# Optimization experiments

Hardware: AMD Instinct MI355X
Metric: run time of the kernel (lower is better)

The kernel has to match this reference:

```python
import jax, jax.numpy as jnp
import numpy as np

C = 66  # channels (joints)
NB_CLASSES = 14
T = 96


def conv1d(x, w, b, pad, groups=1):
    # x: (N, Cin, L), w: (Cout, Cin//groups, K)
    y = jax.lax.conv_general_dilated(
        x, w, window_strides=(1,), padding=[(pad, pad)],
        feature_group_count=groups, dimension_numbers=('NCH', 'OIH', 'NCH'))
    return y + b[None, :, None]


def pool2(x):
    # AvgPool1d(kernel_size=2) along last axis
    return x.reshape(*x.shape[:-1], x.shape[-1] // 2, 2).mean(-1)


def setup_inputs() -> dict:
    key = jax.random.key(0)
    ks = jax.random.split(key, 16)

    def xavier(k, shape, fan_in, fan_out, gain=jnp.sqrt(2.0)):
        bound = gain * jnp.sqrt(6.0 / (fan_in + fan_out))
        return jax.random.uniform(k, shape, jnp.float32, -bound, bound)

    B = 2048
    x = jax.random.normal(ks[0], (B, T, C), jnp.float32)
    # shared convs (same weights for every channel)
    w_hs = xavier(ks[1], (8, 1, 7), 1 * 7, 8 * 7)
    b_hs = jnp.full((8,), 0.1, jnp.float32)
    w_ls = xavier(ks[2], (8, 1, 3), 1 * 3, 8 * 3)
    b_ls = jnp.full((8,), 0.1, jnp.float32)
    # per-channel individual convs, packed for grouped conv (groups=C)
    w_hi1 = xavier(ks[3], (C * 4, 8, 7), 8 * 7, 4 * 7)
    b_hi1 = jnp.full((C * 4,), 0.1, jnp.float32)
    w_hi2 = xavier(ks[4], (C * 4, 4, 7), 4 * 7, 4 * 7)
    b_hi2 = jnp.full((C * 4,), 0.1, jnp.float32)
    w_li1 = xavier(ks[5], (C * 4, 8, 3), 8 * 3, 4 * 3)
    b_li1 = jnp.full((C * 4,), 0.1, jnp.float32)
    w_li2 = xavier(ks[6], (C * 4, 4, 3), 4 * 3, 4 * 3)
    b_li2 = jnp.full((C * 4,), 0.1, jnp.float32)
    # MLP
    F_IN = 9 * C * 12
    w_fc1 = xavier(ks[7], (1936, F_IN), F_IN, 1936)
    b_fc1 = jnp.full((1936,), 0.1, jnp.float32)
    w_fc2 = xavier(ks[8], (NB_CLASSES, 1936), 1936, NB_CLASSES)
    b_fc2 = jnp.full((NB_CLASSES,), 0.1, jnp.float32)
    return dict(x=x, w_hs=w_hs, b_hs=b_hs, w_ls=w_ls, b_ls=b_ls,
                w_hi1=w_hi1, b_hi1=b_hi1, w_hi2=w_hi2, b_hi2=b_hi2,
                w_li1=w_li1, b_li1=b_li1, w_li2=w_li2, b_li2=b_li2,
                w_fc1=w_fc1, b_fc1=b_fc1, w_fc2=w_fc2, b_fc2=b_fc2)


def _branch(xc_flat, B, w_s, b_s, w_i1, b_i1, w_i2, b_i2, pad):
    # xc_flat: (B*C, 1, T). Shared conv applied per channel, then grouped
    # (per-channel) convs with groups=C.
    h = pool2(jax.nn.relu(conv1d(xc_flat, w_s, b_s, pad)))       # (B*C, 8, 48)
    h = h.reshape(B, C * 8, T // 2)
    h = pool2(jax.nn.relu(conv1d(h, w_i1, b_i1, pad, groups=C)))  # (B, C*4, 24)
    h = pool2(jax.nn.relu(conv1d(h, w_i2, b_i2, pad, groups=C)))  # (B, C*4, 12)
    return h.reshape(B, C, 4, T // 8)


def reference(x, w_hs, b_hs, w_ls, b_ls, w_hi1, b_hi1, w_hi2, b_hi2,
              w_li1, b_li1, w_li2, b_li2, w_fc1, b_fc1, w_fc2, b_fc2):
    B = x.shape[0]
    xc = jnp.transpose(x, (0, 2, 1))            # (B, C, T)
    xc_flat = xc.reshape(B * C, 1, T)
    high = _branch(xc_flat, B, w_hs, b_hs, w_hi1, b_hi1, w_hi2, b_hi2, pad=3)
    low = _branch(xc_flat, B, w_ls, b_ls, w_li1, b_li1, w_li2, b_li2, pad=1)
    orig = pool2(pool2(pool2(xc)))[:, :, None, :]  # (B, C, 1, 12)
    # per-channel concat order: [original, low, high] -> (B, C, 9, 12)
    feat = jnp.concatenate([orig, low, high], axis=2).reshape(B, 9 * C * 12)
    h = jax.nn.relu(feat @ w_fc1.T + b_fc1)
    return h @ w_fc2.T + b_fc2
```

## Files before the change

kernel.cpp:

```cpp
#include <hip/hip_runtime.h>
#include <hip/hip_bf16.h>

#define T_LEN 96
#define C_CH  66
#define FIN   7128
#define KPAD  7168
#define NFC1  1936
#define NPAD  2048
#define NCLS  14

typedef __bf16 bf16x8 __attribute__((ext_vector_type(8)));
typedef float  f32x4  __attribute__((ext_vector_type(4)));

#define GLD_LDS(gp, lp) __builtin_amdgcn_global_load_lds(                     \
    (__attribute__((address_space(1))) void*)(gp),                            \
    (__attribute__((address_space(3))) void*)(lp), 16, 0, 0)

__global__ __launch_bounds__(256) void transpose_kernel(
    const float* __restrict__ x, float* __restrict__ xT, int B)
{
    __shared__ float tile[64][65];
    const int t = threadIdx.x & 63;
    const int w = threadIdx.x >> 6;
    const int tc0 = blockIdx.x * 64;
    const int b0  = blockIdx.y * 64;
    #pragma unroll
    for (int j = 0; j < 16; j++) {
        const int r = w * 16 + j;
        tile[r][t] = x[(size_t)(b0 + r) * (T_LEN * C_CH) + tc0 + t];
    }
    __syncthreads();
    #pragma unroll
    for (int j = 0; j < 16; j++) {
        const int r = w * 16 + j;
        xT[(size_t)(tc0 + r) * B + b0 + t] = tile[t][r];
    }
}

__global__ __launch_bounds__(256) void pad_w_kernel(
    const float* __restrict__ w, __hip_bfloat16* __restrict__ wb)
{
    int idx = blockIdx.x * 256 + threadIdx.x;
    int row = idx / 896;
    int cc  = idx - row * 896;
    float4 a = {0.f, 0.f, 0.f, 0.f}, b = {0.f, 0.f, 0.f, 0.f};
    if (row < NFC1 && cc < 891) {
        const float4* src = (const float4*)(w + (size_t)row * FIN + cc * 8);
        a = src[0];
        b = src[1];
    }
    __align__(16) __hip_bfloat16 v[8];
    v[0] = __float2bfloat16(a.x); v[1] = __float2bfloat16(a.y);
    v[2] = __float2bfloat16(a.z); v[3] = __float2bfloat16(a.w);
    v[4] = __float2bfloat16(b.x); v[5] = __float2bfloat16(b.y);
    v[6] = __float2bfloat16(b.z); v[7] = __float2bfloat16(b.w);
    *(int4*)(wb + (size_t)row * KPAD + cc * 8) = *(const int4*)v;
}

template <int K, bool DO_EXTRA>
__device__ __forceinline__ void conv_branch(
    const float* __restrict__ xb, int ts,
    const float* __restrict__ wS, const float* __restrict__ bS,
    const float* __restrict__ wi1, const float* __restrict__ bi1,
    const float* __restrict__ wi2, const float* __restrict__ bi2,
    __hip_bfloat16* __restrict__ frow, int out_off)
{
    constexpr int PAD = K / 2;
    constexpr int XW  = 24 + 6 * PAD;
    constexpr int THW = 12 + 2 * PAD;

    float s2phR[4][24];

    #pragma unroll
    for (int tt = 0; tt < 4; tt++) {
        float xw[XW];
        #pragma unroll
        for (int i = 0; i < XW; i++) {
            const int t = 24 * tt - 3 * PAD + i;
            xw[i] = (t >= 0 && t < T_LEN) ? xb[(size_t)t * ts] : 0.f;
        }

        if (DO_EXTRA) {
            #pragma unroll
            for (int r = 0; r < 3; r++) {
                float s = 0.f;
                #pragma unroll
                for (int k = 0; k < 8; k++) s += xw[3 * PAD + 8 * r + k];
                frow[3 * tt + r] = __float2bfloat16(s * 0.125f);
            }
        }

        float s2a[4][12];
        #pragma unroll
        for (int oc = 0; oc < 4; oc++) {
            const float bv = bi1[oc];
            #pragma unroll
            for (int q = 0; q < 12; q++) s2a[oc][q] = bv;
        }

        #pragma unroll 1
        for (int ic = 0; ic < 8; ic++) {
            const float bs1 = bS[ic];
            float thw[THW];
            #pragma unroll
            for (int j = 0; j < THW; j++) {
                const int jg = 12 * tt - PAD + j;
                if (jg < 0 || jg >= 48) { thw[j] = 0.f; continue; }
                float y0 = bs1, y1 = bs1;
                #pragma unroll
                for (int k = 0; k < K; k++) {
                    const float w = wS[ic * K + k];
                    y0 = fmaf(w, xw[2 * j + k], y0);
                    y1 = fmaf(w, xw[2 * j + 1 + k], y1);
                }
                thw[j] = 0.5f * (fmaxf(y0, 0.f) + fmaxf(y1, 0.f));
            }
            #pragma unroll
            for (int q = 0; q < 12; q++) {
                #pragma unroll
                for (int oc = 0; oc < 4; oc++) {
                    float a = s2a[oc][q];
                    #pragma unroll
                    for (int k = 0; k < K; k++)
                        a = fmaf(wi1[(oc * 8 + ic) * K + k], thw[q + k], a);
                    s2a[oc][q] = a;
                }
            }
        }

        #pragma unroll
        for (int oc = 0; oc < 4; oc++)
            #pragma unroll
            for (int r = 0; r < 6; r++)
                s2phR[oc][6 * tt + r] =
                    0.5f * (fmaxf(s2a[oc][2 * r], 0.f) +
                            fmaxf(s2a[oc][2 * r + 1], 0.f));
    }

    #pragma unroll 1
    for (int oc = 0; oc < 4; oc++) {
        const float bv = bi2[oc];
        #pragma unroll
        for (int q = 0; q < 12; q++) {
            float y0 = bv, y1 = bv;
            #pragma unroll
            for (int ic = 0; ic < 4; ic++) {
                #pragma unroll
                for (int k = 0; k < K; k++) {
                    const float w = wi2[(oc * 4 + ic) * K + k];
                    const int i0 = 2 * q + k - PAD;
                    const int i1 = 2 * q + 1 + k - PAD;
                    if (i0 >= 0 && i0 < 24) y0 = fmaf(w, s2phR[ic][i0], y0);
                    if (i1 >= 0 && i1 < 24) y1 = fmaf(w, s2phR[ic][i1], y1);
                }
            }
            frow[out_off + oc * 12 + q] =
                __float2bfloat16(0.5f * (fmaxf(y0, 0.f) + fmaxf(y1, 0.f)));
        }
    }
}

__global__ __launch_bounds__(64, 2) void conv_fused_kernel(
    const float* __restrict__ x, int ts, int bs, int cs,
    const float* __restrict__ w_hs, const float* __restrict__ b_hs,
    const float* __restrict__ w_ls, const float* __restrict__ b_ls,
    const float* __restrict__ w_hi1, const float* __restrict__ b_hi1,
    const float* __restrict__ w_hi2, const float* __restrict__ b_hi2,
    const float* __restrict__ w_li1, const float* __restrict__ b_li1,
    const float* __restrict__ w_li2, const float* __restrict__ b_li2,
    __hip_bfloat16* __restrict__ feat)
{
    const int lane = threadIdx.x;
    const int b = blockIdx.x * 64 + lane;
    const int c = blockIdx.y;
    const float* xb = x + (size_t)b * bs + (size_t)c * cs;
    __hip_bfloat16* frow = feat + (size_t)b * KPAD + c * 108;

    if (blockIdx.z == 0) {
        conv_branch<7, false>(xb, ts, w_hs, b_hs,
                              w_hi1 + c * 224, b_hi1 + c * 4,
                              w_hi2 + c * 112, b_hi2 + c * 4, frow, 60);
    } else {
        if (c == 0) {
            int4* tail = (int4*)(feat + (size_t)b * KPAD + FIN);
            const int4 z = {0, 0, 0, 0};
            #pragma unroll
            for (int i = 0; i < 5; i++) tail[i] = z;
        }
        conv_branch<3, true>(xb, ts, w_ls, b_ls,
                             w_li1 + c * 96, b_li1 + c * 4,
                             w_li2 + c * 48, b_li2 + c * 4, frow, 12);
    }
}

__global__ __launch_bounds__(256) void gemm_kernel(
    const __hip_bfloat16* __restrict__ A,
    const __hip_bfloat16* __restrict__ Bw,
    float* __restrict__ Cm, int kchunk)
{
    __shared__ __align__(16) __hip_bfloat16 As[4096];
    __shared__ __align__(16) __hip_bfloat16 Bs[4096];

    const int tid  = threadIdx.x;
    const int lane = tid & 63;
    const int wid  = tid >> 6;
    const int m0 = blockIdx.y * 128;
    const int n0 = blockIdx.x * 128;
    const int wm = (wid >> 1) * 64;
    const int wn = (wid & 1) * 64;
    const int lr = lane & 15;
    const int quad = lane >> 4;

    const int r0 = tid >> 2, c0 = (tid & 3) * 8;
    const __hip_bfloat16* gA0 = A  + (size_t)(m0 + r0) * KPAD + c0;
    const __hip_bfloat16* gA1 = gA0 + (size_t)64 * KPAD;
    const __hip_bfloat16* gB0 = Bw + (size_t)(n0 + r0) * KPAD + c0;
    const __hip_bfloat16* gB1 = gB0 + (size_t)64 * KPAD;
    __hip_bfloat16* lA0 = As + wid * 512;
    __hip_bfloat16* lA1 = As + 2048 + wid * 512;
    __hip_bfloat16* lB0 = Bs + wid * 512;
    __hip_bfloat16* lB1 = Bs + 2048 + wid * 512;

    f32x4 acc[4][4] = {};

    const int kBeg = blockIdx.z * kchunk;
    const int kEnd = kBeg + kchunk;
    for (int k0 = kBeg; k0 < kEnd; k0 += 32) {
        __syncthreads();
        GLD_LDS(gA0 + k0, lA0);
        GLD_LDS(gA1 + k0, lA1);
        GLD_LDS(gB0 + k0, lB0);
        GLD_LDS(gB1 + k0, lB1);
        __syncthreads();
        bf16x8 af[4], bfr[4];
        #pragma unroll
        for (int mt = 0; mt < 4; mt++)
            af[mt] = *(const bf16x8*)(As + (wm + mt * 16 + lr) * 32 + quad * 8);
        #pragma unroll
        for (int nt = 0; nt < 4; nt++)
            bfr[nt] = *(const bf16x8*)(Bs + (wn + nt * 16 + lr) * 32 + quad * 8);
        #pragma unroll
        for (int mt = 0; mt < 4; mt++)
            #pragma unroll
            for (int nt = 0; nt < 4; nt++)
                acc[mt][nt] = __builtin_amdgcn_mfma_f32_16x16x32_bf16(
                    af[mt], bfr[nt], acc[mt][nt], 0, 0, 0);
    }

    float* Cs = Cm + (size_t)blockIdx.z * NPAD * NPAD;
    #pragma unroll
    for (int mt = 0; mt < 4; mt++) {
        #pragma unroll
        for (int nt = 0; nt < 4; nt++) {
            const int col = n0 + wn + nt * 16 + lr;
            const int rb  = m0 + wm + mt * 16 + quad * 4;
            #pragma unroll
            for (int r = 0; r < 4; r++)
                Cs[(size_t)(rb + r) * NPAD + col] = acc[mt][nt][r];
        }
    }
}

__global__ __launch_bounds__(256) void fc2_kernel(
    const float* __restrict__ h1, const float* __restrict__ b1,
    const float* __restrict__ w2, const float* __restrict__ b2,
    float* __restrict__ out, int nslab)
{
    const int b = blockIdx.x;
    const int tid = threadIdx.x;
    float acc[NCLS];
    #pragma unroll
    for (int o = 0; o < NCLS; o++) acc[o] = 0.f;
    for (int n = tid; n < NFC1; n += 256) {
        float hv = b1[n];
        for (int s = 0; s < nslab; s++)
            hv += h1[(size_t)s * NPAD * NPAD + (size_t)b * NPAD + n];
        float h = fmaxf(hv, 0.f);
        #pragma unroll
        for (int o = 0; o < NCLS; o++)
            acc[o] = fmaf(h, w2[o * NFC1 + n], acc[o]);
    }
    __shared__ float red[4][NCLS];
    #pragma unroll
    for (int o = 0; o < NCLS; o++) {
        float v = acc[o];
        #pragma unroll
        for (int s = 32; s > 0; s >>= 1) v += __shfl_down(v, s);
        if ((tid & 63) == 0) red[tid >> 6][o] = v;
    }
    __syncthreads();
    if (tid < NCLS)
        out[b * NCLS + tid] = red[0][tid] + red[1][tid] + red[2][tid] +
                              red[3][tid] + b2[tid];
}

extern "C" void kernel_launch(void* const* d_in, const int* in_sizes, int n_in,
                              void* d_out, int out_size, void* d_ws, size_t ws_size,
                              hipStream_t stream)
{
    (void)n_in; (void)out_size;
    const float* x     = (const float*)d_in[0];
    const float* w_hs  = (const float*)d_in[1];
    const float* b_hs  = (const float*)d_in[2];
    const float* w_ls  = (const float*)d_in[3];
    const float* b_ls  = (const float*)d_in[4];
    const float* w_hi1 = (const float*)d_in[5];
    const float* b_hi1 = (const float*)d_in[6];
    const float* w_hi2 = (const float*)d_in[7];
    const float* b_hi2 = (const float*)d_in[8];
    const float* w_li1 = (const float*)d_in[9];
    const float* b_li1 = (const float*)d_in[10];
    const float* w_li2 = (const float*)d_in[11];
    const float* b_li2 = (const float*)d_in[12];
    const float* w_fc1 = (const float*)d_in[13];
    const float* b_fc1 = (const float*)d_in[14];
    const float* w_fc2 = (const float*)d_in[15];
    const float* b_fc2 = (const float*)d_in[16];
    float* out = (float*)d_out;

    const int B = in_sizes[0] / (T_LEN * C_CH);

    char* ws = (char*)d_ws;
    const size_t featB = (size_t)B * KPAD * 2;
    const size_t wbB   = (size_t)NPAD * KPAD * 2;
    const size_t slabB = (size_t)NPAD * NPAD * 4;
    const size_t xtB   = (size_t)T_LEN * C_CH * B * 4;
    const size_t base2 = featB + wbB;

    __hip_bfloat16* feat = (__hip_bfloat16*)ws;
    __hip_bfloat16* wb   = (__hip_bfloat16*)(ws + featB);
    float* h1            = (float*)(ws + base2);

    const int sk = (ws_size >= base2 + 4 * slabB) ? 4 : 2;
    const bool use_xt = (ws_size >= base2 + sk * slabB + xtB);
    float* xT = (float*)(ws + base2 + sk * slabB);

    pad_w_kernel<<<dim3((NPAD * 896) / 256), 256, 0, stream>>>(w_fc1, wb);

    const float* cx = x;
    int ts = C_CH, bsi = T_LEN * C_CH, cs = 1;
    if (use_xt) {
        transpose_kernel<<<dim3(99, B / 64), 256, 0, stream>>>(x, xT, B);
        cx = xT; ts = C_CH * B; bsi = 1; cs = B;
    }
    conv_fused_kernel<<<dim3(B / 64, C_CH, 2), 64, 0, stream>>>(
        cx, ts, bsi, cs, w_hs, b_hs, w_ls, b_ls,
        w_hi1, b_hi1, w_hi2, b_hi2, w_li1, b_li1, w_li2, b_li2, feat);
    gemm_kernel<<<dim3(NPAD / 128, B / 128, sk), 256, 0, stream>>>(
        feat, wb, h1, KPAD / sk);
    fc2_kernel<<<dim3(B), 256, 0, stream>>>(h1, b_fc1, w_fc2, b_fc2, out, sk);
}
```

Before: 431.2 us.

## Stream conv stage-3 over sliding window and split branches into separate kernels

The fused conv kernel is split into two templated kernels, one per branch (K=7 and K=3), each launched separately with launch bounds raised to 3 blocks per SIMD. The time loop now processes 12-sample tiles and computes the final conv/pool stage incrementally from a small sliding window of stage-2 outputs, instead of buffering the full 4x24 intermediate array. This is meant to reduce register pressure and raise occupancy, and to give each kernel a specialized code path without the blockIdx.z branch. The cost is more halo recomputation from smaller tiles, an extra kernel launch, and a reworked pooling pairing that adds correctness risk.

```diff
diff --git a/kernel.cpp b/kernel.cpp
--- a/kernel.cpp
+++ b/kernel.cpp
@@ -58,138 +58,146 @@
 }
 
 template <int K, bool DO_EXTRA>
-__device__ __forceinline__ void conv_branch(
-    const float* __restrict__ xb, int ts,
+__global__ __launch_bounds__(64, 3) void conv_kernel(
+    const float* __restrict__ x, int ts, int bs, int cs,
     const float* __restrict__ wS, const float* __restrict__ bS,
-    const float* __restrict__ wi1, const float* __restrict__ bi1,
-    const float* __restrict__ wi2, const float* __restrict__ bi2,
-    __hip_bfloat16* __restrict__ frow, int out_off)
+    const float* __restrict__ wI1, const float* __restrict__ bI1,
+    const float* __restrict__ wI2, const float* __restrict__ bI2,
+    __hip_bfloat16* __restrict__ feat, int out_off)
 {
     constexpr int PAD = K / 2;
-    constexpr int XW  = 24 + 6 * PAD;
-    constexpr int THW = 12 + 2 * PAD;
-
-    float s2phR[4][24];
-
-    #pragma unroll
-    for (int tt = 0; tt < 4; tt++) {
-        float xw[XW];
-        #pragma unroll
-        for (int i = 0; i < XW; i++) {
-            const int t = 24 * tt - 3 * PAD + i;
-            xw[i] = (t >= 0 && t < T_LEN) ? xb[(size_t)t * ts] : 0.f;
-        }
-
-        if (DO_EXTRA) {
-            #pragma unroll
-            for (int r = 0; r < 3; r++) {
-                float s = 0.f;
-                #pragma unroll
-                for (int k = 0; k < 8; k++) s += xw[3 * PAD + 8 * r + k];
-                frow[3 * tt + r] = __float2bfloat16(s * 0.125f);
-            }
-        }
-
-        float s2a[4][12];
-        #pragma unroll
-        for (int oc = 0; oc < 4; oc++) {
-            const float bv = bi1[oc];
-            #pragma unroll
-            for (int q = 0; q < 12; q++) s2a[oc][q] = bv;
-        }
-
-        #pragma unroll 1
-        for (int ic = 0; ic < 8; ic++) {
-            const float bs1 = bS[ic];
-            float thw[THW];
-            #pragma unroll
-            for (int j = 0; j < THW; j++) {
-                const int jg = 12 * tt - PAD + j;
-                if (jg < 0 || jg >= 48) { thw[j] = 0.f; continue; }
-                float y0 = bs1, y1 = bs1;
-                #pragma unroll
-                for (int k = 0; k < K; k++) {
-                    const float w = wS[ic * K + k];
-                    y0 = fmaf(w, xw[2 * j + k], y0);
-                    y1 = fmaf(w, xw[2 * j + 1 + k], y1);
-                }
-                thw[j] = 0.5f * (fmaxf(y0, 0.f) + fmaxf(y1, 0.f));
-            }
-            #pragma unroll
-            for (int q = 0; q < 12; q++) {
-                #pragma unroll
-                for (int oc = 0; oc < 4; oc++) {
-                    float a = s2a[oc][q];
-                    #pragma unroll
-                    for (int k = 0; k < K; k++)
-                        a = fmaf(wi1[(oc * 8 + ic) * K + k], thw[q + k], a);
-                    s2a[oc][q] = a;
-                }
-            }
-        }
-
-        #pragma unroll
-        for (int oc = 0; oc < 4; oc++)
-            #pragma unroll
-            for (int r = 0; r < 6; r++)
-                s2phR[oc][6 * tt + r] =
-                    0.5f * (fmaxf(s2a[oc][2 * r], 0.f) +
-                            fmaxf(s2a[oc][2 * r + 1], 0.f));
-    }
-
-    #pragma unroll 1
-    for (int oc = 0; oc < 4; oc++) {
-        const float bv = bi2[oc];
-        #pragma unroll
-        for (int q = 0; q < 12; q++) {
-            float y0 = bv, y1 = bv;
-            #pragma unroll
-            for (int ic = 0; ic < 4; ic++) {
-                #pragma unroll
-                for (int k = 0; k < K; k++) {
-                    const float w = wi2[(oc * 4 + ic) * K + k];
-                    const int i0 = 2 * q + k - PAD;
-                    const int i1 = 2 * q + 1 + k - PAD;
-                    if (i0 >= 0 && i0 < 24) y0 = fmaf(w, s2phR[ic][i0], y0);
-                    if (i1 >= 0 && i1 < 24) y1 = fmaf(w, s2phR[ic][i1], y1);
-                }
-            }
-            frow[out_off + oc * 12 + q] =
-                __float2bfloat16(0.5f * (fmaxf(y0, 0.f) + fmaxf(y1, 0.f)));
-        }
-    }
-}
-
-__global__ __launch_bounds__(64, 2) void conv_fused_kernel(
-    const float* __restrict__ x, int ts, int bs, int cs,
-    const float* __restrict__ w_hs, const float* __restrict__ b_hs,
-    const float* __restrict__ w_ls, const float* __restrict__ b_ls,
-    const float* __restrict__ w_hi1, const float* __restrict__ b_hi1,
-    const float* __restrict__ w_hi2, const float* __restrict__ b_hi2,
-    const float* __restrict__ w_li1, const float* __restrict__ b_li1,
-    const float* __restrict__ w_li2, const float* __restrict__ b_li2,
-    __hip_bfloat16* __restrict__ feat)
-{
+    constexpr int XW  = 12 + 6 * PAD;
+    constexpr int THW = 6 + 2 * PAD;
+    constexpr int W   = 3 + 2 * PAD;
+
     const int lane = threadIdx.x;
     const int b = blockIdx.x * 64 + lane;
     const int c = blockIdx.y;
     const float* xb = x + (size_t)b * bs + (size_t)c * cs;
     __hip_bfloat16* frow = feat + (size_t)b * KPAD + c * 108;
 
-    if (blockIdx.z == 0) {
-        conv_branch<7, false>(xb, ts, w_hs, b_hs,
-                              w_hi1 + c * 224, b_hi1 + c * 4,
-                              w_hi2 + c * 112, b_hi2 + c * 4, frow, 60);
-    } else {
+    const float* wi1 = wI1 + c * (4 * 8 * K);
+    const float* bi1 = bI1 + c * 4;
+    const float* wi2 = wI2 + c * (4 * 4 * K);
+    const float* bi2 = bI2 + c * 4;
+
+    if (DO_EXTRA) {
+        #pragma unroll
+        for (int q = 0; q < 12; q++) {
+            float s = 0.f;
+            #pragma unroll
+            for (int k = 0; k < 8; k++) s += xb[(size_t)(q * 8 + k) * ts];
+            frow[q] = __float2bfloat16(s * 0.125f);
+        }
         if (c == 0) {
             int4* tail = (int4*)(feat + (size_t)b * KPAD + FIN);
             const int4 z = {0, 0, 0, 0};
             #pragma unroll
             for (int i = 0; i < 5; i++) tail[i] = z;
         }
-        conv_branch<3, true>(xb, ts, w_ls, b_ls,
-                             w_li1 + c * 96, b_li1 + c * 4,
-                             w_li2 + c * 48, b_li2 + c * 4, frow, 12);
+    }
+
+    float s2w[4][W];
+    float pend[4] = {0.f, 0.f, 0.f, 0.f};
+
+    #pragma unroll
+    for (int tt = 0; tt <= 8; tt++) {
+        if (tt < 8) {
+            float xw[XW];
+            #pragma unroll
+            for (int i = 0; i < XW; i++) {
+                const int t = 12 * tt - 3 * PAD + i;
+                xw[i] = (t >= 0 && t < T_LEN) ? xb[(size_t)t * ts] : 0.f;
+            }
+
+            float s2a[4][6];
+            #pragma unroll
+            for (int oc = 0; oc < 4; oc++) {
+                const float bv = bi1[oc];
+                #pragma unroll
+                for (int q = 0; q < 6; q++) s2a[oc][q] = bv;
+            }
+
+            #pragma unroll 1
+            for (int ic = 0; ic < 8; ic++) {
+                const float bs1 = bS[ic];
+                float thw[THW];
+                #pragma unroll
+                for (int j = 0; j < THW; j++) {
+                    const int jg = 6 * tt - PAD + j;
+                    if (jg < 0 || jg >= 48) { thw[j] = 0.f; continue; }
+                    float y0 = bs1, y1 = bs1;
+                    #pragma unroll
+                    for (int k = 0; k < K; k++) {
+                        const float w = wS[ic * K + k];
+                        y0 = fmaf(w, xw[2 * j + k], y0);
+                        y1 = fmaf(w, xw[2 * j + 1 + k], y1);
+                    }
+                    thw[j] = 0.5f * (fmaxf(y0, 0.f) + fmaxf(y1, 0.f));
+                }
+                #pragma unroll
+                for (int q = 0; q < 6; q++) {
+                    #pragma unroll
+                    for (int oc = 0; oc < 4; oc++) {
+                        float a = s2a[oc][q];
+                        #pragma unroll
+                        for (int k = 0; k < K; k++)
+                            a = fmaf(wi1[(oc * 8 + ic) * K + k], thw[q + k], a);
+                        s2a[oc][q] = a;
+                    }
+                }
+            }
+
+            #pragma unroll
+            for (int ch = 0; ch < 4; ch++) {
+                #pragma unroll
+                for (int i = 0; i < W - 3; i++)
+                    s2w[ch][i] = (tt == 0) ? 0.f : s2w[ch][i + 3];
+                #pragma unroll
+                for (int r = 0; r < 3; r++)
+                    s2w[ch][W - 3 + r] =
+                        0.5f * (fmaxf(s2a[ch][2 * r], 0.f) +
+                                fmaxf(s2a[ch][2 * r + 1], 0.f));
+            }
+        } else {
+            #pragma unroll
+            for (int ch = 0; ch < 4; ch++) {
+                #pragma unroll
+                for (int i = 0; i < W - 3; i++) s2w[ch][i] = s2w[ch][i + 3];
+                #pragma unroll
+                for (int r = 0; r < 3; r++) s2w[ch][W - 3 + r] = 0.f;
+            }
+        }
+
+        #pragma unroll
+        for (int r = 0; r < 3; r++) {
+            const int po = 3 * tt - PAD + r;
+            if (po < 0 || po >= 24) continue;
+            float y[4];
+            #pragma unroll
+            for (int oc = 0; oc < 4; oc++) y[oc] = bi2[oc];
+            #pragma unroll
+            for (int ch = 0; ch < 4; ch++) {
+                #pragma unroll
+                for (int k = 0; k < K; k++) {
+                    const int g = po - PAD + k;
+                    if (g < 0 || g >= 24) continue;
+                    const float v = s2w[ch][r + k];
+                    #pragma unroll
+                    for (int oc = 0; oc < 4; oc++)
+                        y[oc] = fmaf(wi2[(oc * 4 + ch) * K + k], v, y[oc]);
+                }
+            }
+            if ((po & 1) == 0) {
+                #pragma unroll
+                for (int oc = 0; oc < 4; oc++) pend[oc] = fmaxf(y[oc], 0.f);
+            } else {
+                #pragma unroll
+                for (int oc = 0; oc < 4; oc++)
+                    frow[out_off + oc * 12 + (po >> 1)] = __float2bfloat16(
+                        0.5f * (pend[oc] + fmaxf(y[oc], 0.f)));
+            }
+        }
     }
 }
 
@@ -343,9 +351,10 @@
         transpose_kernel<<<dim3(99, B / 64), 256, 0, stream>>>(x, xT, B);
         cx = xT; ts = C_CH * B; bsi = 1; cs = B;
     }
-    conv_fused_kernel<<<dim3(B / 64, C_CH, 2), 64, 0, stream>>>(
-        cx, ts, bsi, cs, w_hs, b_hs, w_ls, b_ls,
-        w_hi1, b_hi1, w_hi2, b_hi2, w_li1, b_li1, w_li2, b_li2, feat);
+    conv_kernel<7, false><<<dim3(B / 64, C_CH), 64, 0, stream>>>(
+        cx, ts, bsi, cs, w_hs, b_hs, w_hi1, b_hi1, w_hi2, b_hi2, feat, 60);
+    conv_kernel<3, true><<<dim3(B / 64, C_CH), 64, 0, stream>>>(
+        cx, ts, bsi, cs, w_ls, b_ls, w_li1, b_li1, w_li2, b_li2, feat, 12);
     gemm_kernel<<<dim3(NPAD / 128, B / 128, sk), 256, 0, stream>>>(
         feat, wb, h1, KPAD / sk);
     fc2_kernel<<<dim3(B), 256, 0, stream>>>(h1, b_fc1, w_fc2, b_fc2, out, sk);
```

Result: slower. 503.2 us (+16.7%).
